# Kernel optimization log

Hardware: AMD Instinct MI355X
Metric: run time of the kernel (lower is better)

The kernel has to match this reference:

```python
import jax, jax.numpy as jnp
import numpy as np

LN_EPS = 1e-6
L2_EPS = 1e-12


def _l2_normalize(v):
    # tf.nn.l2_normalize: v * rsqrt(max(sum(v^2), eps))
    ss = jnp.sum(v * v, axis=-1, keepdims=True)
    return v * jax.lax.rsqrt(jnp.maximum(ss, L2_EPS))


def setup_inputs() -> dict:
    key = jax.random.key(0)
    k1, k2, k3 = jax.random.split(key, 3)
    B, S, D, V = 4, 2048, 1024, 16384
    x = jax.random.normal(k1, (B, S, D), dtype=jnp.float32)
    dict_w = jax.random.normal(k2, (V, D), dtype=jnp.float32) * (2.0 / (V + D)) ** 0.5  # glorot_normal
    ln_gamma = jnp.ones((D,), dtype=jnp.float32)
    ln_beta = jnp.zeros((D,), dtype=jnp.float32)
    o_w = jax.random.normal(k3, (D, D), dtype=jnp.float32) * (2.0 / (D + D)) ** 0.5
    return {"x": x, "dict_w": dict_w, "ln_gamma": ln_gamma, "ln_beta": ln_beta, "o_w": o_w}


def reference(x, dict_w, ln_gamma, ln_beta, o_w):
    # cosine-sim codebook lookup
    q = _l2_normalize(x)                      # [B,S,D]
    k = _l2_normalize(dict_w)                 # [V,D]
    sim = jnp.einsum('bsd,vd->bsv', q, k)     # [B,S,V]
    word_idx = jnp.argmax(sim, axis=-1)       # [B,S] int
    word_sim = jnp.max(sim, axis=-1)          # [B,S]
    z = dict_w[word_idx]                      # gather codebook rows [B,S,D]
    # straight-through estimator
    e = jax.lax.stop_gradient(z - x) + x
    # layernorm (eps=1e-6)
    mu = jnp.mean(e, axis=-1, keepdims=True)
    var = jnp.mean(jnp.square(e - mu), axis=-1, keepdims=True)
    e_ln = (e - mu) * jax.lax.rsqrt(var + LN_EPS) * ln_gamma + ln_beta
    # output projection (no bias)
    out = jnp.einsum('bsd,de->bse', e_ln, o_w)
    return word_idx, word_sim, out
```

## Files before the change

kernel.cpp:

```cpp
#include <hip/hip_runtime.h>
#include <math.h>

#define D 1024
#define V 16384
#define NROWS 8192
#define NCAND 256
#define DELTA 0.15f

typedef __bf16 bf16_t;
typedef bf16_t bf16x8 __attribute__((ext_vector_type(8)));
typedef float f32x4 __attribute__((ext_vector_type(4)));
typedef int i32x4 __attribute__((ext_vector_type(4)));

__device__ __forceinline__ unsigned int sortable_key(float v) {
    unsigned int b = __float_as_uint(v);
    return (b & 0x80000000u) ? ~b : (b | 0x80000000u);
}
__device__ __forceinline__ float unkey(unsigned int key) {
    unsigned int b = (key & 0x80000000u) ? (key & 0x7FFFFFFFu) : ~key;
    return __uint_as_float(b);
}
__device__ __forceinline__ void split4(float4 v, uint2& hw, uint2& lw) {
    unsigned int u0 = __float_as_uint(v.x), u1 = __float_as_uint(v.y);
    unsigned int u2 = __float_as_uint(v.z), u3 = __float_as_uint(v.w);
    float l0 = v.x - __uint_as_float(u0 & 0xFFFF0000u);
    float l1 = v.y - __uint_as_float(u1 & 0xFFFF0000u);
    float l2 = v.z - __uint_as_float(u2 & 0xFFFF0000u);
    float l3 = v.w - __uint_as_float(u3 & 0xFFFF0000u);
    hw.x = (u0 >> 16) | (u1 & 0xFFFF0000u);
    hw.y = (u2 >> 16) | (u3 & 0xFFFF0000u);
    lw.x = (__float_as_uint(l0) >> 16) | (__float_as_uint(l1) & 0xFFFF0000u);
    lw.y = (__float_as_uint(l2) >> 16) | (__float_as_uint(l3) & 0xFFFF0000u);
}

__device__ __forceinline__ void gload16(const unsigned char* g, unsigned char* s) {
    __builtin_amdgcn_global_load_lds((const __attribute__((address_space(1))) void*)g,
                                     (__attribute__((address_space(3))) void*)s,
                                     16, 0, 0);
}

__global__ __launch_bounds__(256) void prep_kernel(const float* __restrict__ W,
                                                   const float* __restrict__ X,
                                                   float* __restrict__ RK,
                                                   float* __restrict__ RQ,
                                                   float* __restrict__ SA,
                                                   float* __restrict__ SB,
                                                   float* __restrict__ RKS,
                                                   unsigned long long* __restrict__ packed,
                                                   unsigned int* __restrict__ count) {
    int tid = threadIdx.x;
    int row = blockIdx.x * 4 + (tid >> 6);
    int lane = tid & 63;
    const float* src = (row < V) ? (W + (size_t)row * D) : (X + (size_t)(row - V) * D);
    const float4* p = (const float4*)src;
    float ss = 0.f, am = 0.f;
#pragma unroll
    for (int i = 0; i < 4; ++i) {
        float4 v = p[lane + 64 * i];
        ss += v.x * v.x + v.y * v.y + v.z * v.z + v.w * v.w;
        am = fmaxf(am, fmaxf(fmaxf(fabsf(v.x), fabsf(v.y)), fmaxf(fabsf(v.z), fabsf(v.w))));
    }
#pragma unroll
    for (int m = 32; m >= 1; m >>= 1) {
        ss += __shfl_xor(ss, m, 64);
        am = fmaxf(am, __shfl_xor(am, m, 64));
    }
    if (lane == 0) {
        float rk = rsqrtf(fmaxf(ss, 1e-12f));
        float s = am * (1.f / 127.f);
        if (row < V) {
            RK[row] = rk;
            SB[row] = s;
            RKS[row] = rk * s;
        } else {
            RQ[row - V] = rk;
            SA[row - V] = s;
            packed[row - V] = 0ull;
            count[row - V] = 0u;
        }
    }
}

__global__ __launch_bounds__(256) void pack_i8_kernel(const float* __restrict__ src,
                                                      const float* __restrict__ S,
                                                      unsigned char* __restrict__ dst) {
    int tid = threadIdx.x;
    int row = blockIdx.x;
    int k0 = tid * 4;
    float4 v = *((const float4*)(src + (size_t)row * D) + tid);
    float s = S[row];
    float inv = (s > 0.f) ? (1.f / s) : 0.f;
    int q0 = (int)rintf(v.x * inv), q1 = (int)rintf(v.y * inv);
    int q2 = (int)rintf(v.z * inv), q3 = (int)rintf(v.w * inv);
    q0 = q0 > 127 ? 127 : (q0 < -127 ? -127 : q0);
    q1 = q1 > 127 ? 127 : (q1 < -127 ? -127 : q1);
    q2 = q2 > 127 ? 127 : (q2 < -127 ? -127 : q2);
    q3 = q3 > 127 ? 127 : (q3 < -127 ? -127 : q3);
    unsigned int word = (unsigned int)(q0 & 0xFF) | ((unsigned int)(q1 & 0xFF) << 8) |
                        ((unsigned int)(q2 & 0xFF) << 16) | ((unsigned int)(q3 & 0xFF) << 24);
    int kc = k0 >> 6, kk = k0 & 63;
    int lane = (row & 15) | ((kk >> 4) << 4);
    int j0 = kk & 15;
    size_t idx = ((size_t)(row >> 4) * 16 + kc) * 1024 + lane * 16 + j0;
    *(unsigned int*)(dst + idx) = word;
}

__global__ __launch_bounds__(256, 4) void gemm1_kernel(const unsigned char* __restrict__ Xq,
                                                       const unsigned char* __restrict__ Wq,
                                                       const float* __restrict__ SA,
                                                       const float* __restrict__ RKS,
                                                       unsigned long long* __restrict__ packed,
                                                       unsigned int* __restrict__ count,
                                                       ushort* __restrict__ candCol,
                                                       int colBase, int perX) {
    __shared__ __align__(16) unsigned char lds[32768];
    __shared__ unsigned long long red[128][2];
    __shared__ float gthr[128];

    const int tid = threadIdx.x;
    const int l = tid & 63;
    const int w = tid >> 6;
    const int wy = w >> 1, wx = w & 1;
    const int lin = blockIdx.x;
    const int x = lin & 7;
    const int j = lin >> 3;
    const int rt = j / perX;
    const int ctl = x * perX + (j - rt * perX);
    const int rowBase = rt * 128;
    const int cwLocal = ctl * 128;

    i32x4 acc[4][4];
#pragma unroll
    for (int mt = 0; mt < 4; ++mt)
#pragma unroll
        for (int nt = 0; nt < 4; ++nt) acc[mt][nt] = (i32x4)0;

    const unsigned char* As = Xq + ((size_t)(rt * 8) * 16) * 1024;
    const unsigned char* Bs = Wq + ((size_t)((colBase >> 4) + ctl * 8) * 16) * 1024;

#pragma unroll 1
    for (int kc = 0; kc < 16; kc += 2) {
#pragma unroll
        for (int i = 0; i < 2; ++i) {
            int u = 2 * w + i;
#pragma unroll
            for (int jj = 0; jj < 2; ++jj) {
                gload16(As + ((size_t)(u * 16 + kc + jj)) * 1024 + l * 16,
                        lds + (u * 2 + jj) * 1024);
                gload16(Bs + ((size_t)(u * 16 + kc + jj)) * 1024 + l * 16,
                        lds + 16384 + (u * 2 + jj) * 1024);
            }
        }
        __syncthreads();
#pragma unroll
        for (int jj = 0; jj < 2; ++jj) {
            i32x4 af[4], bf[4];
#pragma unroll
            for (int mi = 0; mi < 4; ++mi)
                af[mi] = *(const i32x4*)(lds + ((wy * 4 + mi) * 2 + jj) * 1024 + l * 16);
#pragma unroll
            for (int nt = 0; nt < 4; ++nt)
                bf[nt] = *(const i32x4*)(lds + 16384 + ((wx * 4 + nt) * 2 + jj) * 1024 + l * 16);
#pragma unroll
            for (int nt = 0; nt < 4; ++nt)
#pragma unroll
                for (int mi = 0; mi < 4; ++mi)
                    acc[mi][nt] = __builtin_amdgcn_mfma_i32_16x16x64_i8(af[mi], bf[nt], acc[mi][nt], 0, 0, 0);
        }
        __syncthreads();
    }

    const int q = l >> 4, c = l & 15;
    float rk_l[4];
#pragma unroll
    for (int nt = 0; nt < 4; ++nt) rk_l[nt] = RKS[colBase + cwLocal + wx * 64 + nt * 16 + c];
#pragma unroll
    for (int mt = 0; mt < 4; ++mt) {
#pragma unroll
        for (int r = 0; r < 4; ++r) {
            float sa = SA[rowBase + wy * 64 + mt * 16 + q * 4 + r];
            unsigned long long pk = 0;
#pragma unroll
            for (int nt = 0; nt < 4; ++nt) {
                float v = (float)acc[mt][nt][r] * sa * rk_l[nt];
                int col = colBase + cwLocal + wx * 64 + nt * 16 + c;
                unsigned long long p = ((unsigned long long)sortable_key(v) << 32) |
                                       (unsigned long long)(~(unsigned int)col);
                if (p > pk) pk = p;
            }
#pragma unroll
            for (int m = 1; m < 16; m <<= 1) {
                unsigned long long o = __shfl_xor(pk, m, 64);
                if (o > pk) pk = o;
            }
            if (c == 0) red[wy * 64 + mt * 16 + q * 4 + r][wx] = pk;
        }
    }
    __syncthreads();
    if (tid < 128) {
        unsigned long long a = red[tid][0], bb = red[tid][1];
        if (bb > a) a = bb;
        unsigned long long old = atomicMax(packed + (rowBase + tid), a);
        unsigned long long g = (old > a) ? old : a;
        gthr[tid] = unkey((unsigned int)(g >> 32)) - DELTA;
    }
    __syncthreads();
#pragma unroll
    for (int mt = 0; mt < 4; ++mt) {
#pragma unroll
        for (int r = 0; r < 4; ++r) {
            int lrow = wy * 64 + mt * 16 + q * 4 + r;
            float thr = gthr[lrow];
            int grow = rowBase + lrow;
            float sa = SA[grow];
#pragma unroll
            for (int nt = 0; nt < 4; ++nt) {
                float v = (float)acc[mt][nt][r] * sa * rk_l[nt];
                if (v >= thr) {
                    unsigned int slot = atomicAdd(count + grow, 1u);
                    if (slot < NCAND) {
                        int col = colBase + cwLocal + wx * 64 + nt * 16 + c;
                        candCol[(size_t)grow * NCAND + slot] = (ushort)col;
                    }
                }
            }
        }
    }
}

__global__ __launch_bounds__(256) void rescore_kernel(const float* __restrict__ X,
                                                      const float* __restrict__ W,
                                                      const float* __restrict__ RK,
                                                      const float* __restrict__ RQ,
                                                      const unsigned int* __restrict__ count,
                                                      const ushort* __restrict__ candCol,
                                                      float* __restrict__ outIdx,
                                                      float* __restrict__ outSim,
                                                      int* __restrict__ idxArr,
                                                      float* __restrict__ MU,
                                                      float* __restrict__ RS) {
    int wave = threadIdx.x >> 6, l = threadIdx.x & 63;
    int row = blockIdx.x * 4 + wave;
    unsigned int n = count[row];
    if (n > NCAND) n = NCAND;
    const float4* X4 = (const float4*)X + (size_t)row * 256;
    unsigned long long best = 0;
    for (unsigned int i = 0; i < n; ++i) {
        int col = (int)candCol[(size_t)row * NCAND + i];
        const float4* W4 = (const float4*)W + (size_t)col * 256;
        float s = 0.f;
#pragma unroll
        for (int jj = 0; jj < 4; ++jj) {
            float4 a = X4[jj * 64 + l];
            float4 b = W4[jj * 64 + l];
            s += a.x * b.x + a.y * b.y + a.z * b.z + a.w * b.w;
        }
#pragma unroll
        for (int m = 32; m >= 1; m >>= 1) s += __shfl_xor(s, m, 64);
        float v = s * RK[col];
        unsigned long long pk = ((unsigned long long)sortable_key(v) << 32) |
                                (unsigned long long)(~(unsigned int)col);
        if (pk > best) best = pk;
    }
    int idx = (int)(~(unsigned int)(best & 0xFFFFFFFFull)) & 0xFFFF;
    const float4* Z4 = (const float4*)W + (size_t)idx * 256;
    float s = 0.f, s2 = 0.f;
#pragma unroll
    for (int jj = 0; jj < 4; ++jj) {
        float4 a = X4[jj * 64 + l];
        float4 z = Z4[jj * 64 + l];
        float4 e;
        e.x = (z.x - a.x) + a.x;
        e.y = (z.y - a.y) + a.y;
        e.z = (z.z - a.z) + a.z;
        e.w = (z.w - a.w) + a.w;
        s  += e.x + e.y + e.z + e.w;
        s2 += e.x * e.x + e.y * e.y + e.z * e.z + e.w * e.w;
    }
#pragma unroll
    for (int m = 32; m >= 1; m >>= 1) {
        s  += __shfl_xor(s, m, 64);
        s2 += __shfl_xor(s2, m, 64);
    }
    if (l == 0) {
        outIdx[row] = (float)idx;
        outSim[row] = unkey((unsigned int)(best >> 32)) * RQ[row];
        idxArr[row] = idx;
        float mean = s * (1.f / D);
        float var  = s2 * (1.f / D) - mean * mean;
        MU[row] = mean;
        RS[row] = rsqrtf(var + 1e-6f);
    }
}

__global__ __launch_bounds__(256, 2) void gemm2_kernel(const float* __restrict__ X,
                                                       const float* __restrict__ W,
                                                       const int* __restrict__ idxArr,
                                                       const float* __restrict__ MU,
                                                       const float* __restrict__ RS,
                                                       const float* __restrict__ gamma,
                                                       const float* __restrict__ beta,
                                                       const float* __restrict__ B,
                                                       float* __restrict__ Out) {
    __shared__ ushort Ah[2][8][64][8];
    __shared__ ushort Al[2][8][64][8];
    __shared__ ushort Bh2[2][8][64][8];
    __shared__ ushort Bl2[2][8][64][8];
    __shared__ float Gs[1024];
    __shared__ float Bt[1024];

    const int tid = threadIdx.x;
    const int l = tid & 63;
    const int wave = tid >> 6;
    const int wy = wave >> 1, wx = wave & 1;
    const int rowBase = blockIdx.y * 128;
    const int nBase   = blockIdx.x * 128;

    *(float4*)&Gs[tid * 4] = *(const float4*)(gamma + tid * 4);
    *(float4*)&Bt[tid * 4] = *(const float4*)(beta + tid * 4);

    f32x4 acc[4][4];
#pragma unroll
    for (int mt = 0; mt < 4; ++mt)
#pragma unroll
        for (int nt = 0; nt < 4; ++nt) acc[mt][nt] = (f32x4)0.f;

    const int srow = tid >> 3, skq = tid & 7;
    const int sn = tid & 127, sdq = tid >> 7;
    int aidx[4];
    float amu[4], ars[4];
#pragma unroll
    for (int i = 0; i < 4; ++i) {
        int grow = rowBase + srow + i * 32;
        aidx[i] = idxArr[grow];
        amu[i] = MU[grow];
        ars[i] = RS[grow];
    }

    __syncthreads();

    float4 pz[4], pxv[4], pbv[4];
#pragma unroll
    for (int i = 0; i < 4; ++i) {
        int col = skq * 4;
        pz[i]  = *(const float4*)(W + (size_t)aidx[i] * D + col);
        pxv[i] = *(const float4*)(X + (size_t)(rowBase + srow + i * 32) * D + col);
    }
#pragma unroll
    for (int i = 0; i < 4; ++i) {
        const float* bp = B + (size_t)((sdq + i * 2) * 4) * D + nBase + sn;
        pbv[i] = {bp[0], bp[D], bp[2 * D], bp[3 * D]};
    }

    for (int kc = 0; kc < 32; ++kc) {
        const int bsel = kc & 1;
#pragma unroll
        for (int i = 0; i < 4; ++i) {
            int row = srow + i * 32;
            int col = kc * 32 + skq * 4;
            float4 z = pz[i], xv = pxv[i];
            float4 g  = *(const float4*)&Gs[col];
            float4 bb = *(const float4*)&Bt[col];
            float4 a;
            a.x = (((z.x - xv.x) + xv.x) - amu[i]) * ars[i] * g.x + bb.x;
            a.y = (((z.y - xv.y) + xv.y) - amu[i]) * ars[i] * g.y + bb.y;
            a.z = (((z.z - xv.z) + xv.z) - amu[i]) * ars[i] * g.z + bb.z;
            a.w = (((z.w - xv.w) + xv.w) - amu[i]) * ars[i] * g.w + bb.w;
            uint2 hw, lw;
            split4(a, hw, lw);
            int tile = row >> 4;
            int lf = (row & 15) | ((skq >> 1) << 4);
            int j0 = (skq & 1) * 4;
            *(uint2*)&Ah[bsel][tile][lf][j0] = hw;
            *(uint2*)&Al[bsel][tile][lf][j0] = lw;
        }
#pragma unroll
        for (int i = 0; i < 4; ++i) {
            int dq = sdq + i * 2;
            uint2 hw, lw;
            split4(pbv[i], hw, lw);
            int tile = sn >> 4;
            int lf = (sn & 15) | ((dq >> 1) << 4);
            int j0 = (dq & 1) * 4;
            *(uint2*)&Bh2[bsel][tile][lf][j0] = hw;
            *(uint2*)&Bl2[bsel][tile][lf][j0] = lw;
        }
        __syncthreads();
        float4 pzn[4], pxvn[4], pbvn[4];
        if (kc < 31) {
#pragma unroll
            for (int i = 0; i < 4; ++i) {
                int col = (kc + 1) * 32 + skq * 4;
                pzn[i]  = *(const float4*)(W + (size_t)aidx[i] * D + col);
                pxvn[i] = *(const float4*)(X + (size_t)(rowBase + srow + i * 32) * D + col);
            }
#pragma unroll
            for (int i = 0; i < 4; ++i) {
                const float* bp = B + (size_t)((kc + 1) * 32 + (sdq + i * 2) * 4) * D + nBase + sn;
                pbvn[i] = {bp[0], bp[D], bp[2 * D], bp[3 * D]};
            }
        }
        bf16x8 fah[4], fal[4];
#pragma unroll
        for (int mt = 0; mt < 4; ++mt) {
            fah[mt] = *(const bf16x8*)&Ah[bsel][wy * 4 + mt][l][0];
            fal[mt] = *(const bf16x8*)&Al[bsel][wy * 4 + mt][l][0];
        }
#pragma unroll
        for (int nt = 0; nt < 4; ++nt) {
            bf16x8 bh = *(const bf16x8*)&Bh2[bsel][wx * 4 + nt][l][0];
            bf16x8 bl = *(const bf16x8*)&Bl2[bsel][wx * 4 + nt][l][0];
#pragma unroll
            for (int mt = 0; mt < 4; ++mt) {
                acc[mt][nt] = __builtin_amdgcn_mfma_f32_16x16x32_bf16(fah[mt], bh, acc[mt][nt], 0, 0, 0);
                acc[mt][nt] = __builtin_amdgcn_mfma_f32_16x16x32_bf16(fah[mt], bl, acc[mt][nt], 0, 0, 0);
                acc[mt][nt] = __builtin_amdgcn_mfma_f32_16x16x32_bf16(fal[mt], bh, acc[mt][nt], 0, 0, 0);
            }
        }
        if (kc < 31) {
#pragma unroll
            for (int i = 0; i < 4; ++i) {
                pz[i] = pzn[i]; pxv[i] = pxvn[i]; pbv[i] = pbvn[i];
            }
        }
    }

    const int q = l >> 4, c = l & 15;
#pragma unroll
    for (int mt = 0; mt < 4; ++mt)
#pragma unroll
        for (int nt = 0; nt < 4; ++nt)
#pragma unroll
            for (int r = 0; r < 4; ++r) {
                int grow = rowBase + wy * 64 + mt * 16 + q * 4 + r;
                int gcol = nBase + wx * 64 + nt * 16 + c;
                Out[(size_t)grow * D + gcol] = acc[mt][nt][r];
            }
}

extern "C" void kernel_launch(void* const* d_in, const int* in_sizes, int n_in,
                              void* d_out, int out_size, void* d_ws, size_t ws_size,
                              hipStream_t stream) {
    const float* X     = (const float*)d_in[0];
    const float* W     = (const float*)d_in[1];
    const float* gamma = (const float*)d_in[2];
    const float* beta  = (const float*)d_in[3];
    const float* OW    = (const float*)d_in[4];

    float* out    = (float*)d_out;
    float* outIdx = out;
    float* outSim = out + NROWS;
    float* outO   = out + 2 * NROWS;

    unsigned char* Xq8 = (unsigned char*)outO;
    unsigned char* Wq8 = Xq8 + (size_t)NROWS * D;
    ushort* candCol = (ushort*)(Wq8 + (size_t)V * D);
    unsigned int* count = (unsigned int*)(candCol + (size_t)NROWS * NCAND);
    float* SA  = (float*)(count + NROWS);
    float* SB  = SA + NROWS;
    float* RKS = SB + V;

    unsigned long long* packed = (unsigned long long*)d_ws;
    float* RK     = (float*)(packed + NROWS);
    float* RQ     = RK + V;
    float* MU     = RQ + NROWS;
    float* RS     = MU + NROWS;
    int*   idxArr = (int*)(RS + NROWS);

    hipLaunchKernelGGL(prep_kernel, dim3((V + NROWS) / 4), dim3(256), 0, stream,
                       W, X, RK, RQ, SA, SB, RKS, packed, count);
    hipLaunchKernelGGL(pack_i8_kernel, dim3(NROWS), dim3(256), 0, stream, X, SA, Xq8);
    hipLaunchKernelGGL(pack_i8_kernel, dim3(V), dim3(256), 0, stream, W, SB, Wq8);

    for (int ch = 0; ch < 2; ++ch) {
        int colBase = ch * 8192;
        int perX = (8192 / 128) / 8;
        hipLaunchKernelGGL(gemm1_kernel, dim3((NROWS / 128) * (8192 / 128)), dim3(256), 0, stream,
                           Xq8, Wq8, SA, RKS, packed, count, candCol, colBase, perX);
    }

    hipLaunchKernelGGL(rescore_kernel, dim3(NROWS / 4), dim3(256), 0, stream,
                       X, W, RK, RQ, count, candCol, outIdx, outSim, idxArr, MU, RS);
    hipLaunchKernelGGL(gemm2_kernel, dim3(D / 128, NROWS / 128), dim3(256), 0, stream,
                       X, W, idxArr, MU, RS, gamma, beta, OW, outO);
}
```

Baseline: 527.1 us.

## Widen int8 similarity GEMM tile to 128x256 and simplify row-max reduction

```diff
diff --git a/kernel.cpp b/kernel.cpp
--- a/kernel.cpp
+++ b/kernel.cpp
@@ -46,7 +46,7 @@
                                                    float* __restrict__ SA,
                                                    float* __restrict__ SB,
                                                    float* __restrict__ RKS,
-                                                   unsigned long long* __restrict__ packed,
+                                                   unsigned int* __restrict__ packed,
                                                    unsigned int* __restrict__ count) {
     int tid = threadIdx.x;
     int row = blockIdx.x * 4 + (tid >> 6);
@@ -75,7 +75,7 @@
         } else {
             RQ[row - V] = rk;
             SA[row - V] = s;
-            packed[row - V] = 0ull;
+            packed[row - V] = 0u;
             count[row - V] = 0u;
         }
     }
@@ -105,16 +105,16 @@
     *(unsigned int*)(dst + idx) = word;
 }
 
-__global__ __launch_bounds__(256, 4) void gemm1_kernel(const unsigned char* __restrict__ Xq,
+__global__ __launch_bounds__(256, 2) void gemm1_kernel(const unsigned char* __restrict__ Xq,
                                                        const unsigned char* __restrict__ Wq,
                                                        const float* __restrict__ SA,
                                                        const float* __restrict__ RKS,
-                                                       unsigned long long* __restrict__ packed,
+                                                       unsigned int* __restrict__ packed,
                                                        unsigned int* __restrict__ count,
                                                        ushort* __restrict__ candCol,
                                                        int colBase, int perX) {
-    __shared__ __align__(16) unsigned char lds[32768];
-    __shared__ unsigned long long red[128][2];
+    __shared__ __align__(16) unsigned char lds[49152];
+    __shared__ float red[128][2];
     __shared__ float gthr[128];
 
     const int tid = threadIdx.x;
@@ -127,16 +127,16 @@
     const int rt = j / perX;
     const int ctl = x * perX + (j - rt * perX);
     const int rowBase = rt * 128;
-    const int cwLocal = ctl * 128;
-
-    i32x4 acc[4][4];
+    const int cwLocal = ctl * 256;
+
+    i32x4 acc[4][8];
 #pragma unroll
     for (int mt = 0; mt < 4; ++mt)
 #pragma unroll
-        for (int nt = 0; nt < 4; ++nt) acc[mt][nt] = (i32x4)0;
+        for (int nt = 0; nt < 8; ++nt) acc[mt][nt] = (i32x4)0;
 
     const unsigned char* As = Xq + ((size_t)(rt * 8) * 16) * 1024;
-    const unsigned char* Bs = Wq + ((size_t)((colBase >> 4) + ctl * 8) * 16) * 1024;
+    const unsigned char* Bs = Wq + ((size_t)((colBase >> 4) + ctl * 16) * 16) * 1024;
 
 #pragma unroll 1
     for (int kc = 0; kc < 16; kc += 2) {
@@ -144,25 +144,30 @@
         for (int i = 0; i < 2; ++i) {
             int u = 2 * w + i;
 #pragma unroll
-            for (int jj = 0; jj < 2; ++jj) {
+            for (int jj = 0; jj < 2; ++jj)
                 gload16(As + ((size_t)(u * 16 + kc + jj)) * 1024 + l * 16,
                         lds + (u * 2 + jj) * 1024);
+        }
+#pragma unroll
+        for (int i = 0; i < 4; ++i) {
+            int u = 4 * w + i;
+#pragma unroll
+            for (int jj = 0; jj < 2; ++jj)
                 gload16(Bs + ((size_t)(u * 16 + kc + jj)) * 1024 + l * 16,
                         lds + 16384 + (u * 2 + jj) * 1024);
-            }
         }
         __syncthreads();
 #pragma unroll
         for (int jj = 0; jj < 2; ++jj) {
-            i32x4 af[4], bf[4];
+            i32x4 af[4], bf[8];
 #pragma unroll
             for (int mi = 0; mi < 4; ++mi)
                 af[mi] = *(const i32x4*)(lds + ((wy * 4 + mi) * 2 + jj) * 1024 + l * 16);
 #pragma unroll
-            for (int nt = 0; nt < 4; ++nt)
-                bf[nt] = *(const i32x4*)(lds + 16384 + ((wx * 4 + nt) * 2 + jj) * 1024 + l * 16);
-#pragma unroll
-            for (int nt = 0; nt < 4; ++nt)
+            for (int nt = 0; nt < 8; ++nt)
+                bf[nt] = *(const i32x4*)(lds + 16384 + ((wx * 8 + nt) * 2 + jj) * 1024 + l * 16);
+#pragma unroll
+            for (int nt = 0; nt < 8; ++nt)
 #pragma unroll
                 for (int mi = 0; mi < 4; ++mi)
                     acc[mi][nt] = __builtin_amdgcn_mfma_i32_16x16x64_i8(af[mi], bf[nt], acc[mi][nt], 0, 0, 0);
@@ -171,38 +176,32 @@
     }
 
     const int q = l >> 4, c = l & 15;
-    float rk_l[4];
-#pragma unroll
-    for (int nt = 0; nt < 4; ++nt) rk_l[nt] = RKS[colBase + cwLocal + wx * 64 + nt * 16 + c];
+    float rk_l[8];
+#pragma unroll
+    for (int nt = 0; nt < 8; ++nt) rk_l[nt] = RKS[colBase + cwLocal + wx * 128 + nt * 16 + c];
 #pragma unroll
     for (int mt = 0; mt < 4; ++mt) {
 #pragma unroll
         for (int r = 0; r < 4; ++r) {
-            float sa = SA[rowBase + wy * 64 + mt * 16 + q * 4 + r];
-            unsigned long long pk = 0;
-#pragma unroll
-            for (int nt = 0; nt < 4; ++nt) {
-                float v = (float)acc[mt][nt][r] * sa * rk_l[nt];
-                int col = colBase + cwLocal + wx * 64 + nt * 16 + c;
-                unsigned long long p = ((unsigned long long)sortable_key(v) << 32) |
-                                       (unsigned long long)(~(unsigned int)col);
-                if (p > pk) pk = p;
-            }
-#pragma unroll
-            for (int m = 1; m < 16; m <<= 1) {
-                unsigned long long o = __shfl_xor(pk, m, 64);
-                if (o > pk) pk = o;
-            }
-            if (c == 0) red[wy * 64 + mt * 16 + q * 4 + r][wx] = pk;
+            int lrow = wy * 64 + mt * 16 + q * 4 + r;
+            float sa = SA[rowBase + lrow];
+            float vmax = -1e30f;
+#pragma unroll
+            for (int nt = 0; nt < 8; ++nt)
+                vmax = fmaxf(vmax, (float)acc[mt][nt][r] * sa * rk_l[nt]);
+#pragma unroll
+            for (int m = 1; m < 16; m <<= 1)
+                vmax = fmaxf(vmax, __shfl_xor(vmax, m, 64));
+            if (c == 0) red[lrow][wx] = vmax;
         }
     }
     __syncthreads();
     if (tid < 128) {
-        unsigned long long a = red[tid][0], bb = red[tid][1];
-        if (bb > a) a = bb;
-        unsigned long long old = atomicMax(packed + (rowBase + tid), a);
-        unsigned long long g = (old > a) ? old : a;
-        gthr[tid] = unkey((unsigned int)(g >> 32)) - DELTA;
+        float a = fmaxf(red[tid][0], red[tid][1]);
+        unsigned int k = sortable_key(a);
+        unsigned int old = atomicMax(packed + (rowBase + tid), k);
+        unsigned int g = (old > k) ? old : k;
+        gthr[tid] = unkey(g) - DELTA;
     }
     __syncthreads();
 #pragma unroll
@@ -214,12 +213,12 @@
             int grow = rowBase + lrow;
             float sa = SA[grow];
 #pragma unroll
-            for (int nt = 0; nt < 4; ++nt) {
+            for (int nt = 0; nt < 8; ++nt) {
                 float v = (float)acc[mt][nt][r] * sa * rk_l[nt];
                 if (v >= thr) {
                     unsigned int slot = atomicAdd(count + grow, 1u);
                     if (slot < NCAND) {
-                        int col = colBase + cwLocal + wx * 64 + nt * 16 + c;
+                        int col = colBase + cwLocal + wx * 128 + nt * 16 + c;
                         candCol[(size_t)grow * NCAND + slot] = (ushort)col;
                     }
                 }
@@ -460,7 +459,7 @@
     float* SB  = SA + NROWS;
     float* RKS = SB + V;
 
-    unsigned long long* packed = (unsigned long long*)d_ws;
+    unsigned int* packed = (unsigned int*)d_ws;
     float* RK     = (float*)(packed + NROWS);
     float* RQ     = RK + V;
     float* MU     = RQ + NROWS;
@@ -474,8 +473,8 @@
 
     for (int ch = 0; ch < 2; ++ch) {
         int colBase = ch * 8192;
-        int perX = (8192 / 128) / 8;
-        hipLaunchKernelGGL(gemm1_kernel, dim3((NROWS / 128) * (8192 / 128)), dim3(256), 0, stream,
+        int perX = (8192 / 256) / 8;
+        hipLaunchKernelGGL(gemm1_kernel, dim3((NROWS / 128) * (8192 / 256)), dim3(256), 0, stream,
                            Xq8, Wq8, SA, RKS, packed, count, candCol, colBase, perX);
     }
 
```

New measurement: 499.5 us. 1.06x faster.
